# Performance work log

Measured on AMD Instinct MI355X. Metric: run time of the kernel, lower is better.

Reference implementation:

```python
import jax, jax.numpy as jnp
import numpy as np

TOKENS, HIDDEN, FFN = 4096, 4096, 14336
SCALE = 0.02  # keep activations in a sane range


def setup_inputs() -> dict:
    key = jax.random.key(0)
    k1, k2, k3, k4 = jax.random.split(key, 4)
    x = jax.random.normal(k1, (TOKENS, HIDDEN), dtype=jnp.float32)
    expert_w1 = jax.random.normal(k2, (FFN, HIDDEN), dtype=jnp.float32) * SCALE
    expert_v1 = jax.random.normal(k3, (FFN, HIDDEN), dtype=jnp.float32) * SCALE
    expert_w2 = jax.random.normal(k4, (FFN, HIDDEN), dtype=jnp.float32) * SCALE
    return {"x": x, "expert_w1": expert_w1, "expert_v1": expert_v1, "expert_w2": expert_w2}


def reference(x, expert_w1, expert_v1, expert_w2):
    # gate/up projections: [T, H] @ [H, F] -> [T, F]
    gate = jnp.einsum('th,fh->tf', x, expert_w1)
    up = jnp.einsum('th,fh->tf', x, expert_v1)
    inter = jax.nn.silu(gate) * up            # fused SwiGLU intermediate [T, F]
    down = jnp.einsum('tf,fh->th', inter, expert_w2)  # [T, H]
    return down
```

## Files before the change

kernel.cpp:

```cpp
#include <hip/hip_runtime.h>
#include <hip/hip_bf16.h>
#include <stdint.h>

#define TOKENS 4096
#define HIDDEN 4096
#define FFN    14336

typedef __attribute__((ext_vector_type(8))) short bf16x8;
typedef __attribute__((ext_vector_type(4))) float f32x4;
typedef __attribute__((ext_vector_type(8))) unsigned short u16x8;

typedef __attribute__((address_space(3))) void lds_void_t;
typedef const __attribute__((address_space(1))) void gbl_void_t;

static __device__ __forceinline__ unsigned short f2b(float f) {
  union { float f; unsigned int u; } v; v.f = f;
  unsigned int u = v.u;
  return (unsigned short)((u + 0x7FFFu + ((u >> 16) & 1u)) >> 16);
}

__global__ void cvt_kernel(const float* __restrict__ in, unsigned short* __restrict__ out, long n) {
  long idx = (long)blockIdx.x * blockDim.x + threadIdx.x;
  long stride = (long)gridDim.x * blockDim.x;
  for (long i = idx * 4; i < n; i += stride * 4) {
    const float4 v = *reinterpret_cast<const float4*>(in + i);
    ushort4 o;
    o.x = f2b(v.x); o.y = f2b(v.y); o.z = f2b(v.z); o.w = f2b(v.w);
    *reinterpret_cast<ushort4*>(out + i) = o;
  }
}

__global__ void transpose_cvt_kernel(const float* __restrict__ in, unsigned short* __restrict__ out) {
  __shared__ float tile[64][65];
  const int f0 = blockIdx.x * 64;
  const int h0 = blockIdx.y * 64;
  const int t = threadIdx.x;
  const int rcol = (t & 15) * 4;
  const int rrow = t >> 4;
#pragma unroll
  for (int it = 0; it < 4; ++it) {
    int r = rrow + it * 16;
    const float4 v = *reinterpret_cast<const float4*>(in + (long)(f0 + r) * HIDDEN + h0 + rcol);
    tile[r][rcol] = v.x; tile[r][rcol + 1] = v.y; tile[r][rcol + 2] = v.z; tile[r][rcol + 3] = v.w;
  }
  __syncthreads();
  const int wrow = t >> 2;
  const int wc = (t & 3) * 16;
  u16x8 lo, hi;
#pragma unroll
  for (int j = 0; j < 8; ++j) lo[j] = f2b(tile[wc + j][wrow]);
#pragma unroll
  for (int j = 0; j < 8; ++j) hi[j] = f2b(tile[wc + 8 + j][wrow]);
  u16x8* dst = reinterpret_cast<u16x8*>(out + (long)(h0 + wrow) * FFN + f0 + wc);
  dst[0] = lo; dst[1] = hi;
}

#define MFMA16(a, b, c) __builtin_amdgcn_mfma_f32_16x16x32_bf16((a), (b), (c), 0, 0, 0)
#define SBAR()  __builtin_amdgcn_s_barrier()

static __device__ __forceinline__ int xcd_chunk(int bid, int nwg) {
  return (bid & 7) * (nwg >> 3) + (bid >> 3);
}

__global__ __launch_bounds__(512, 2)
void gateup256p_kernel(const unsigned short* __restrict__ X,
                       const unsigned short* __restrict__ W1,
                       const unsigned short* __restrict__ V1,
                       unsigned short* __restrict__ Inter,
                       int j0, int j1) {
  __shared__ unsigned short sh[81920];
  const int tid = threadIdx.x, lane = tid & 63, wid = tid >> 6;
  const int wm = wid >> 2, wn = wid & 3;
  const int p = blockIdx.x;
  const int bm = p & 15;
  const int bnl = p >> 4;
  const int sr = tid >> 3;
  const int scb = (((tid & 7) ^ (sr & 7)) << 4);
  const int l15 = lane & 15;
  const int cb0 = (((lane >> 4) * 16) ^ ((lane & 7) << 4));
  const int cb1 = ((64 + (lane >> 4) * 16) ^ ((lane & 7) << 4));

  const unsigned short* Ap = X + (long)(bm * 256) * HIDDEN;

  auto LDA8 = [&](bf16x8* a, int bufA, int cb) {
    const char* base = (const char*)sh + bufA * 32768 + wm * 16384 + l15 * 128 + cb;
#pragma unroll
    for (int m = 0; m < 8; ++m) a[m] = *(const bf16x8*)(base + m * 2048);
  };
  auto LDW2 = [&](bf16x8* w, int b3, int cb) {
    const char* base = (const char*)sh + 65536 + b3 * 32768 + (wn * 32 + l15) * 128 + cb;
    w[0] = *(const bf16x8*)(base);
    w[1] = *(const bf16x8*)(base + 2048);
  };
  auto LDV2 = [&](bf16x8* v, int b3, int cb) {
    const char* base = (const char*)sh + 65536 + b3 * 32768 + 16384 + (wn * 32 + l15) * 128 + cb;
    v[0] = *(const bf16x8*)(base);
    v[1] = *(const bf16x8*)(base + 2048);
  };

  for (int j = j0; j < j1; ++j) {
    const int bn = j * 16 + bnl;
    const unsigned short* Wp = W1 + (long)(bn * 128) * HIDDEN;
    const unsigned short* Vp = V1 + (long)(bn * 128) * HIDDEN;

    auto STA = [&](int u, int bufA, int t) {
      const unsigned short* src = Ap + (long)(u * 64 + sr) * HIDDEN + t * 64 + (scb >> 1);
      unsigned short* dst = sh + bufA * 16384 + u * 4096 + tid * 8;
      __builtin_amdgcn_global_load_lds((gbl_void_t*)src, (lds_void_t*)dst, 16, 0, 0);
    };
    auto STW = [&](int u, int b3, int t) {
      const unsigned short* src = Wp + (long)(u * 64 + sr) * HIDDEN + t * 64 + (scb >> 1);
      unsigned short* dst = sh + 32768 + b3 * 16384 + u * 4096 + tid * 8;
      __builtin_amdgcn_global_load_lds((gbl_void_t*)src, (lds_void_t*)dst, 16, 0, 0);
    };
    auto STV = [&](int u, int b3, int t) {
      const unsigned short* src = Vp + (long)(u * 64 + sr) * HIDDEN + t * 64 + (scb >> 1);
      unsigned short* dst = sh + 32768 + b3 * 16384 + 8192 + u * 4096 + tid * 8;
      __builtin_amdgcn_global_load_lds((gbl_void_t*)src, (lds_void_t*)dst, 16, 0, 0);
    };

    f32x4 accg[8][2] = {};
    f32x4 accu[8][2] = {};

    STW(0, 0, 0); STW(1, 0, 0); STV(0, 0, 0); STV(1, 0, 0);
    STA(0, 0, 0); STA(1, 0, 0); STA(2, 0, 0); STA(3, 0, 0);
    STW(0, 1, 1); STW(1, 1, 1); STV(0, 1, 1); STV(1, 1, 1);

    bf16x8 a[8], w[2], v[2];
    const int NT = HIDDEN / 64;
    for (int t = 0; t < NT; ++t) {
      const int curA = t & 1, nxtA = curA ^ 1;
      const int b3 = t % 3, b3w = (t + 2) % 3;
      if (t + 1 < NT) { asm volatile("s_waitcnt vmcnt(4)" ::: "memory"); }
      else            { asm volatile("s_waitcnt vmcnt(0)" ::: "memory"); }
      SBAR();
      if (t + 1 < NT) { STA(0, nxtA, t + 1); STA(1, nxtA, t + 1);
                        STA(2, nxtA, t + 1); STA(3, nxtA, t + 1); }
      LDA8(a, curA, cb0); LDW2(w, b3, cb0);
      __builtin_amdgcn_s_setprio(1);
#pragma unroll
      for (int m = 0; m < 8; ++m) {
        accg[m][0] = MFMA16(a[m], w[0], accg[m][0]);
        accg[m][1] = MFMA16(a[m], w[1], accg[m][1]);
      }
      __builtin_amdgcn_s_setprio(0);
      SBAR();
      if (t + 2 < NT) { STW(0, b3w, t + 2); STW(1, b3w, t + 2);
                        STV(0, b3w, t + 2); STV(1, b3w, t + 2); }
      LDV2(v, b3, cb0);
      __builtin_amdgcn_s_setprio(1);
#pragma unroll
      for (int m = 0; m < 8; ++m) {
        accu[m][0] = MFMA16(a[m], v[0], accu[m][0]);
        accu[m][1] = MFMA16(a[m], v[1], accu[m][1]);
      }
      __builtin_amdgcn_s_setprio(0);
      SBAR();
      LDA8(a, curA, cb1); LDW2(w, b3, cb1);
      __builtin_amdgcn_s_setprio(1);
#pragma unroll
      for (int m = 0; m < 8; ++m) {
        accg[m][0] = MFMA16(a[m], w[0], accg[m][0]);
        accg[m][1] = MFMA16(a[m], w[1], accg[m][1]);
      }
      __builtin_amdgcn_s_setprio(0);
      SBAR();
      LDV2(v, b3, cb1);
      __builtin_amdgcn_s_setprio(1);
#pragma unroll
      for (int m = 0; m < 8; ++m) {
        accu[m][0] = MFMA16(a[m], v[0], accu[m][0]);
        accu[m][1] = MFMA16(a[m], v[1], accu[m][1]);
      }
      __builtin_amdgcn_s_setprio(0);
      SBAR();
    }
    const int r0 = (lane >> 4) * 4;
#pragma unroll
    for (int m = 0; m < 8; ++m)
#pragma unroll
      for (int n = 0; n < 2; ++n)
#pragma unroll
        for (int r = 0; r < 4; ++r) {
          const float g = accg[m][n][r];
          const float u = accu[m][n][r];
          const float s = g / (1.0f + __expf(-g));
          const int row = bm * 256 + wm * 128 + m * 16 + r0 + r;
          const int col = bn * 128 + wn * 32 + n * 16 + l15;
          Inter[(long)row * FFN + col] = f2b(s * u);
        }
    asm volatile("s_waitcnt vmcnt(0)" ::: "memory");
  }
}

__global__ __launch_bounds__(512, 2)
void down256_kernel(const unsigned short* __restrict__ Inter,
                    const unsigned short* __restrict__ W2t,
                    float* __restrict__ Out) {
  __shared__ unsigned short sh[65536];
  const int tid = threadIdx.x, lane = tid & 63, wid = tid >> 6;
  const int wm = wid >> 2, wn = wid & 3;
  const int swz = xcd_chunk(blockIdx.x, (TOKENS / 256) * (HIDDEN / 256));
  const int bm = swz & 15;
  const int bn = swz >> 4;
  const int sr = tid >> 3;
  const int scb = (((tid & 7) ^ (sr & 7)) << 4);
  const int l15 = lane & 15;
  const int cb0 = (((lane >> 4) * 16) ^ ((lane & 7) << 4));
  const int cb1 = ((64 + (lane >> 4) * 16) ^ ((lane & 7) << 4));

  const unsigned short* Ap = Inter + (long)(bm * 256) * FFN;
  const unsigned short* Bp = W2t + (long)(bn * 256) * FFN;

  f32x4 acc[8][4] = {};

  auto STAGE = [&](int kind, int h, int buf, int t) {
    const unsigned short* src = (kind ? Bp : Ap) + (long)(h * 128 + sr) * FFN + t * 64 + (scb >> 1);
    unsigned short* dst = sh + buf * 32768 + kind * 16384 + h * 8192 + tid * 8;
    __builtin_amdgcn_global_load_lds((gbl_void_t*)src, (lds_void_t*)dst, 16, 0, 0);
    __builtin_amdgcn_global_load_lds((gbl_void_t*)(src + 64L * FFN), (lds_void_t*)(dst + 4096), 16, 0, 0);
  };
  auto LDA8 = [&](bf16x8* a, int buf, int cb) {
    const char* base = (const char*)sh + buf * 65536 + wm * 16384 + l15 * 128 + cb;
#pragma unroll
    for (int m = 0; m < 8; ++m) a[m] = *(const bf16x8*)(base + m * 2048);
  };
  auto LDB2 = [&](bf16x8* b, int buf, int cb, int np) {
    const char* base = (const char*)sh + buf * 65536 + 32768 + (wn >> 1) * 16384 +
                       ((wn & 1) * 64 + l15) * 128 + cb;
    b[2 * np]     = *(const bf16x8*)(base + (2 * np) * 2048);
    b[2 * np + 1] = *(const bf16x8*)(base + (2 * np + 1) * 2048);
  };

  STAGE(0, 0, 0, 0); STAGE(0, 1, 0, 0); STAGE(1, 0, 0, 0); STAGE(1, 1, 0, 0);

  bf16x8 a[8], b[4];
  const int NT = FFN / 64;
  for (int t = 0; t < NT; ++t) {
    const int cur = t & 1, nxt = cur ^ 1;
    const bool pre = (t + 1 < NT);
    if (pre) { STAGE(1, 0, nxt, t + 1); STAGE(1, 1, nxt, t + 1);
               asm volatile("s_waitcnt vmcnt(4)" ::: "memory"); }
    else     { asm volatile("s_waitcnt vmcnt(0)" ::: "memory"); }
    SBAR();
    LDA8(a, cur, cb0); LDB2(b, cur, cb0, 0);
    __builtin_amdgcn_s_setprio(1);
#pragma unroll
    for (int m = 0; m < 8; ++m) {
      acc[m][0] = MFMA16(a[m], b[0], acc[m][0]);
      acc[m][1] = MFMA16(a[m], b[1], acc[m][1]);
    }
    __builtin_amdgcn_s_setprio(0);
    SBAR();
    if (pre) { STAGE(0, 0, nxt, t + 1); STAGE(0, 1, nxt, t + 1); }
    LDB2(b, cur, cb0, 1);
    __builtin_amdgcn_s_setprio(1);
#pragma unroll
    for (int m = 0; m < 8; ++m) {
      acc[m][2] = MFMA16(a[m], b[2], acc[m][2]);
      acc[m][3] = MFMA16(a[m], b[3], acc[m][3]);
    }
    __builtin_amdgcn_s_setprio(0);
    SBAR();
    LDA8(a, cur, cb1); LDB2(b, cur, cb1, 0);
    __builtin_amdgcn_s_setprio(1);
#pragma unroll
    for (int m = 0; m < 8; ++m) {
      acc[m][0] = MFMA16(a[m], b[0], acc[m][0]);
      acc[m][1] = MFMA16(a[m], b[1], acc[m][1]);
    }
    __builtin_amdgcn_s_setprio(0);
    SBAR();
    LDB2(b, cur, cb1, 1);
    __builtin_amdgcn_s_setprio(1);
#pragma unroll
    for (int m = 0; m < 8; ++m) {
      acc[m][2] = MFMA16(a[m], b[2], acc[m][2]);
      acc[m][3] = MFMA16(a[m], b[3], acc[m][3]);
    }
    __builtin_amdgcn_s_setprio(0);
    SBAR();
  }
  const int r0 = (lane >> 4) * 4;
#pragma unroll
  for (int m = 0; m < 8; ++m)
#pragma unroll
    for (int n = 0; n < 4; ++n)
#pragma unroll
      for (int r = 0; r < 4; ++r) {
        const int row = bm * 256 + wm * 128 + m * 16 + r0 + r;
        const int col = bn * 256 + wn * 64 + n * 16 + l15;
        Out[(long)row * HIDDEN + col] = acc[m][n][r];
      }
}

__device__ __forceinline__ void stage_tile_128(const unsigned short* __restrict__ g, long ldk,
                                               unsigned short* lds, int wave, int lane) {
#pragma unroll
  for (int it = 0; it < 2; ++it) {
    const int row = (it * 4 + wave) * 16 + (lane >> 2);
    const int kcol = (lane & 3) * 8;
    const unsigned short* src = g + (long)row * ldk + kcol;
    unsigned short* dst = lds + row * 32 + kcol;
    __builtin_amdgcn_global_load_lds((gbl_void_t*)src, (lds_void_t*)dst, 16, 0, 0);
  }
}

__global__ __launch_bounds__(256, 2)
void down_nt_kernel(const unsigned short* __restrict__ Inter,
                    const float* __restrict__ W2,
                    float* __restrict__ Out) {
  __shared__ unsigned short As[128 * 32];
  __shared__ unsigned short Bs[128 * 32];
  const int t = threadIdx.x;
  const int lane = t & 63;
  const int wave = t >> 6;
  const int bm = blockIdx.x & 31;
  const int bn = blockIdx.x >> 5;
  const int wm = (wave >> 1) * 64;
  const int wn = (wave & 1) * 64;
  const unsigned short* gA = Inter + (long)(bm * 128) * FFN;

  f32x4 acc[4][4] = {};
  const int fr = lane & 15;
  const int kg = (lane >> 4) * 8;
  const int p = lane & 15;
  const int h0 = wave * 32 + (lane >> 4) * 8;
  const float* gB = W2 + bn * 128 + h0;

  for (int kt = 0; kt < FFN; kt += 32) {
    __syncthreads();
    stage_tile_128(gA + kt, FFN, As, wave, lane);
    const float* r0p = gB + (long)(kt + 2 * p) * HIDDEN;
    const float* r1p = r0p + HIDDEN;
    const float4 a0 = *reinterpret_cast<const float4*>(r0p);
    const float4 a1 = *reinterpret_cast<const float4*>(r0p + 4);
    const float4 b0 = *reinterpret_cast<const float4*>(r1p);
    const float4 b1 = *reinterpret_cast<const float4*>(r1p + 4);
    unsigned short lo[8], hi[8];
    lo[0] = f2b(a0.x); lo[1] = f2b(a0.y); lo[2] = f2b(a0.z); lo[3] = f2b(a0.w);
    lo[4] = f2b(a1.x); lo[5] = f2b(a1.y); lo[6] = f2b(a1.z); lo[7] = f2b(a1.w);
    hi[0] = f2b(b0.x); hi[1] = f2b(b0.y); hi[2] = f2b(b0.z); hi[3] = f2b(b0.w);
    hi[4] = f2b(b1.x); hi[5] = f2b(b1.y); hi[6] = f2b(b1.z); hi[7] = f2b(b1.w);
#pragma unroll
    for (int j = 0; j < 8; ++j) {
      const unsigned int pack = (unsigned int)lo[j] | ((unsigned int)hi[j] << 16);
      *reinterpret_cast<unsigned int*>(&Bs[(h0 + j) * 32 + 2 * p]) = pack;
    }
    __syncthreads();
    bf16x8 a[4], b[4];
#pragma unroll
    for (int m = 0; m < 4; ++m)
      a[m] = *reinterpret_cast<const bf16x8*>(&As[(wm + m * 16 + fr) * 32 + kg]);
#pragma unroll
    for (int n = 0; n < 4; ++n)
      b[n] = *reinterpret_cast<const bf16x8*>(&Bs[(wn + n * 16 + fr) * 32 + kg]);
#pragma unroll
    for (int m = 0; m < 4; ++m)
#pragma unroll
      for (int n = 0; n < 4; ++n)
        acc[m][n] = MFMA16(a[m], b[n], acc[m][n]);
  }
  const int r0 = (lane >> 4) * 4;
#pragma unroll
  for (int m = 0; m < 4; ++m)
#pragma unroll
    for (int n = 0; n < 4; ++n)
#pragma unroll
      for (int r = 0; r < 4; ++r) {
        const int row = bm * 128 + wm + m * 16 + r0 + r;
        const int col = bn * 128 + wn + n * 16 + fr;
        Out[(long)row * HIDDEN + col] = acc[m][n][r];
      }
}

extern "C" void kernel_launch(void* const* d_in, const int* in_sizes, int n_in,
                              void* d_out, int out_size, void* d_ws, size_t ws_size,
                              hipStream_t stream) {
  const float* x  = (const float*)d_in[0];
  const float* w1 = (const float*)d_in[1];
  const float* v1 = (const float*)d_in[2];
  const float* w2 = (const float*)d_in[3];
  float* out = (float*)d_out;

  const size_t REQ_SMALL = 385875968UL;
  const size_t REQ_FULL  = 503316480UL;
  if (ws_size < REQ_SMALL) return;
  const bool full = (ws_size >= REQ_FULL);
  char* ws = (char*)d_ws;
  unsigned short* xb     = (unsigned short*)(ws);
  unsigned short* w1b    = (unsigned short*)(ws + 33554432L);
  unsigned short* v1b    = (unsigned short*)(ws + 150994944L);
  unsigned short* interb = (unsigned short*)(ws + 268435456L);
  unsigned short* w2tb   = (unsigned short*)(ws + 385875968L);

  const long HALF1 = 8192L * HIDDEN;
  const long HALF2 = (long)(FFN - 8192) * HIDDEN;

  hipLaunchKernelGGL(cvt_kernel, dim3(2048), dim3(256), 0, stream, x, xb, (long)TOKENS * HIDDEN);
  hipLaunchKernelGGL(cvt_kernel, dim3(2048), dim3(256), 0, stream, w1, w1b, HALF1);
  hipLaunchKernelGGL(cvt_kernel, dim3(2048), dim3(256), 0, stream, v1, v1b, HALF1);
  hipLaunchKernelGGL(gateup256p_kernel, dim3(256), dim3(512), 0, stream,
                     xb, w1b, v1b, interb, 0, 4);
  hipLaunchKernelGGL(cvt_kernel, dim3(2048), dim3(256), 0, stream, w1 + HALF1, w1b + HALF1, HALF2);
  hipLaunchKernelGGL(cvt_kernel, dim3(2048), dim3(256), 0, stream, v1 + HALF1, v1b + HALF1, HALF2);
  hipLaunchKernelGGL(gateup256p_kernel, dim3(256), dim3(512), 0, stream,
                     xb, w1b, v1b, interb, 4, 7);

  if (full) {
    hipLaunchKernelGGL(transpose_cvt_kernel, dim3(FFN / 64, HIDDEN / 64), dim3(256), 0, stream, w2, w2tb);
    hipLaunchKernelGGL(down256_kernel, dim3((TOKENS / 256) * (HIDDEN / 256)), dim3(512), 0, stream,
                       interb, w2tb, out);
  } else {
    hipLaunchKernelGGL(down_nt_kernel, dim3((TOKENS / 128) * (HIDDEN / 128)), dim3(256), 0, stream,
                       interb, w2, out);
  }
}
```

Measured before the change: 1.395 ms.

## Collapse per-step barriers to one and triple-buffer B tiles in down GEMM

The gate/up loop now issues its W/V prefetch at the top of each k-step, loads W and V fragments together, and synchronises once per step instead of five times. The down GEMM is restructured the same way. A stays double-buffered, B becomes triple-buffered with prefetch two steps ahead, and there is a single lgkmcnt-wait-plus-barrier per iteration. This is meant to cut barrier stalls and let more MFMA work overlap with global-to-LDS loads. The down kernel's LDS grows from 128KB to 160KB, which may stop two 512-thread blocks fitting per CU, and fragment register pressure rises.

```diff
diff --git a/kernel.cpp b/kernel.cpp
--- a/kernel.cpp
+++ b/kernel.cpp
@@ -131,49 +131,40 @@
     for (int t = 0; t < NT; ++t) {
       const int curA = t & 1, nxtA = curA ^ 1;
       const int b3 = t % 3, b3w = (t + 2) % 3;
+      asm volatile("s_waitcnt lgkmcnt(0)" ::: "memory");
       if (t + 1 < NT) { asm volatile("s_waitcnt vmcnt(4)" ::: "memory"); }
       else            { asm volatile("s_waitcnt vmcnt(0)" ::: "memory"); }
       SBAR();
       if (t + 1 < NT) { STA(0, nxtA, t + 1); STA(1, nxtA, t + 1);
                         STA(2, nxtA, t + 1); STA(3, nxtA, t + 1); }
-      LDA8(a, curA, cb0); LDW2(w, b3, cb0);
+      if (t + 2 < NT) { STW(0, b3w, t + 2); STW(1, b3w, t + 2);
+                        STV(0, b3w, t + 2); STV(1, b3w, t + 2); }
+      LDA8(a, curA, cb0); LDW2(w, b3, cb0); LDV2(v, b3, cb0);
       __builtin_amdgcn_s_setprio(1);
 #pragma unroll
       for (int m = 0; m < 8; ++m) {
         accg[m][0] = MFMA16(a[m], w[0], accg[m][0]);
         accg[m][1] = MFMA16(a[m], w[1], accg[m][1]);
       }
-      __builtin_amdgcn_s_setprio(0);
-      SBAR();
-      if (t + 2 < NT) { STW(0, b3w, t + 2); STW(1, b3w, t + 2);
-                        STV(0, b3w, t + 2); STV(1, b3w, t + 2); }
-      LDV2(v, b3, cb0);
-      __builtin_amdgcn_s_setprio(1);
 #pragma unroll
       for (int m = 0; m < 8; ++m) {
         accu[m][0] = MFMA16(a[m], v[0], accu[m][0]);
         accu[m][1] = MFMA16(a[m], v[1], accu[m][1]);
       }
       __builtin_amdgcn_s_setprio(0);
-      SBAR();
-      LDA8(a, curA, cb1); LDW2(w, b3, cb1);
+      LDA8(a, curA, cb1); LDW2(w, b3, cb1); LDV2(v, b3, cb1);
       __builtin_amdgcn_s_setprio(1);
 #pragma unroll
       for (int m = 0; m < 8; ++m) {
         accg[m][0] = MFMA16(a[m], w[0], accg[m][0]);
         accg[m][1] = MFMA16(a[m], w[1], accg[m][1]);
       }
-      __builtin_amdgcn_s_setprio(0);
-      SBAR();
-      LDV2(v, b3, cb1);
-      __builtin_amdgcn_s_setprio(1);
 #pragma unroll
       for (int m = 0; m < 8; ++m) {
         accu[m][0] = MFMA16(a[m], v[0], accu[m][0]);
         accu[m][1] = MFMA16(a[m], v[1], accu[m][1]);
       }
       __builtin_amdgcn_s_setprio(0);
-      SBAR();
     }
     const int r0 = (lane >> 4) * 4;
 #pragma unroll
@@ -197,7 +188,7 @@
 void down256_kernel(const unsigned short* __restrict__ Inter,
                     const unsigned short* __restrict__ W2t,
                     float* __restrict__ Out) {
-  __shared__ unsigned short sh[65536];
+  __shared__ unsigned short sh[81920];
   const int tid = threadIdx.x, lane = tid & 63, wid = tid >> 6;
   const int wm = wid >> 2, wn = wid & 3;
   const int swz = xcd_chunk(blockIdx.x, (TOKENS / 256) * (HIDDEN / 256));
@@ -214,72 +205,71 @@
 
   f32x4 acc[8][4] = {};
 
-  auto STAGE = [&](int kind, int h, int buf, int t) {
-    const unsigned short* src = (kind ? Bp : Ap) + (long)(h * 128 + sr) * FFN + t * 64 + (scb >> 1);
-    unsigned short* dst = sh + buf * 32768 + kind * 16384 + h * 8192 + tid * 8;
+  auto STA = [&](int h, int bufA, int t) {
+    const unsigned short* src = Ap + (long)(h * 128 + sr) * FFN + t * 64 + (scb >> 1);
+    unsigned short* dst = sh + bufA * 16384 + h * 8192 + tid * 8;
     __builtin_amdgcn_global_load_lds((gbl_void_t*)src, (lds_void_t*)dst, 16, 0, 0);
     __builtin_amdgcn_global_load_lds((gbl_void_t*)(src + 64L * FFN), (lds_void_t*)(dst + 4096), 16, 0, 0);
   };
-  auto LDA8 = [&](bf16x8* a, int buf, int cb) {
-    const char* base = (const char*)sh + buf * 65536 + wm * 16384 + l15 * 128 + cb;
+  auto STB = [&](int h, int s3, int t) {
+    const unsigned short* src = Bp + (long)(h * 128 + sr) * FFN + t * 64 + (scb >> 1);
+    unsigned short* dst = sh + 32768 + s3 * 16384 + h * 8192 + tid * 8;
+    __builtin_amdgcn_global_load_lds((gbl_void_t*)src, (lds_void_t*)dst, 16, 0, 0);
+    __builtin_amdgcn_global_load_lds((gbl_void_t*)(src + 64L * FFN), (lds_void_t*)(dst + 4096), 16, 0, 0);
+  };
+  auto LDA8 = [&](bf16x8* a, int bufA, int cb) {
+    const char* base = (const char*)sh + bufA * 32768 + wm * 16384 + l15 * 128 + cb;
 #pragma unroll
     for (int m = 0; m < 8; ++m) a[m] = *(const bf16x8*)(base + m * 2048);
   };
-  auto LDB2 = [&](bf16x8* b, int buf, int cb, int np) {
-    const char* base = (const char*)sh + buf * 65536 + 32768 + (wn >> 1) * 16384 +
+  auto LDB2 = [&](bf16x8* b, int s3, int cb, int np) {
+    const char* base = (const char*)sh + 65536 + s3 * 32768 + (wn >> 1) * 16384 +
                        ((wn & 1) * 64 + l15) * 128 + cb;
     b[2 * np]     = *(const bf16x8*)(base + (2 * np) * 2048);
     b[2 * np + 1] = *(const bf16x8*)(base + (2 * np + 1) * 2048);
   };
 
-  STAGE(0, 0, 0, 0); STAGE(0, 1, 0, 0); STAGE(1, 0, 0, 0); STAGE(1, 1, 0, 0);
+  STB(0, 0, 0); STB(1, 0, 0);
+  STA(0, 0, 0); STA(1, 0, 0);
+  STB(0, 1, 1); STB(1, 1, 1);
 
   bf16x8 a[8], b[4];
   const int NT = FFN / 64;
   for (int t = 0; t < NT; ++t) {
-    const int cur = t & 1, nxt = cur ^ 1;
-    const bool pre = (t + 1 < NT);
-    if (pre) { STAGE(1, 0, nxt, t + 1); STAGE(1, 1, nxt, t + 1);
-               asm volatile("s_waitcnt vmcnt(4)" ::: "memory"); }
-    else     { asm volatile("s_waitcnt vmcnt(0)" ::: "memory"); }
+    const int curA = t & 1, nxtA = curA ^ 1;
+    const int b3 = t % 3, b3w = (t + 2) % 3;
+    asm volatile("s_waitcnt lgkmcnt(0)" ::: "memory");
+    if (t + 1 < NT) { asm volatile("s_waitcnt vmcnt(4)" ::: "memory"); }
+    else            { asm volatile("s_waitcnt vmcnt(0)" ::: "memory"); }
     SBAR();
-    LDA8(a, cur, cb0); LDB2(b, cur, cb0, 0);
+    if (t + 1 < NT) { STA(0, nxtA, t + 1); STA(1, nxtA, t + 1); }
+    if (t + 2 < NT) { STB(0, b3w, t + 2); STB(1, b3w, t + 2); }
+    LDA8(a, curA, cb0); LDB2(b, b3, cb0, 0); LDB2(b, b3, cb0, 1);
     __builtin_amdgcn_s_setprio(1);
 #pragma unroll
     for (int m = 0; m < 8; ++m) {
       acc[m][0] = MFMA16(a[m], b[0], acc[m][0]);
       acc[m][1] = MFMA16(a[m], b[1], acc[m][1]);
     }
-    __builtin_amdgcn_s_setprio(0);
-    SBAR();
-    if (pre) { STAGE(0, 0, nxt, t + 1); STAGE(0, 1, nxt, t + 1); }
-    LDB2(b, cur, cb0, 1);
-    __builtin_amdgcn_s_setprio(1);
 #pragma unroll
     for (int m = 0; m < 8; ++m) {
       acc[m][2] = MFMA16(a[m], b[2], acc[m][2]);
       acc[m][3] = MFMA16(a[m], b[3], acc[m][3]);
     }
     __builtin_amdgcn_s_setprio(0);
-    SBAR();
-    LDA8(a, cur, cb1); LDB2(b, cur, cb1, 0);
+    LDA8(a, curA, cb1); LDB2(b, b3, cb1, 0); LDB2(b, b3, cb1, 1);
     __builtin_amdgcn_s_setprio(1);
 #pragma unroll
     for (int m = 0; m < 8; ++m) {
       acc[m][0] = MFMA16(a[m], b[0], acc[m][0]);
       acc[m][1] = MFMA16(a[m], b[1], acc[m][1]);
     }
-    __builtin_amdgcn_s_setprio(0);
-    SBAR();
-    LDB2(b, cur, cb1, 1);
-    __builtin_amdgcn_s_setprio(1);
 #pragma unroll
     for (int m = 0; m < 8; ++m) {
       acc[m][2] = MFMA16(a[m], b[2], acc[m][2]);
       acc[m][3] = MFMA16(a[m], b[3], acc[m][3]);
     }
     __builtin_amdgcn_s_setprio(0);
-    SBAR();
   }
   const int r0 = (lane >> 4) * 4;
 #pragma unroll
```

Result: no change. 1.369 ms (-1.9%).
